# Performance work log

Hardware: AMD Instinct MI355X
Metric: run time of the kernel (lower is better)

## Reference

```python
import jax, jax.numpy as jnp
import numpy as np

D_MODEL = 1024
HEADS = 16
D_K = D_MODEL // HEADS
B, S = 2, 2048


def setup_inputs() -> dict:
    key = jax.random.key(0)
    ks = jax.random.split(key, 11)
    sc = 1.0 / np.sqrt(D_MODEL)
    return {
        "q": jax.random.normal(ks[0], (B, S, D_MODEL), jnp.float32),
        "k": jax.random.normal(ks[1], (B, S, D_MODEL), jnp.float32),
        "v": jax.random.normal(ks[2], (B, S, D_MODEL), jnp.float32),
        "Wq": jax.random.normal(ks[3], (D_MODEL, D_MODEL), jnp.float32) * sc,
        "bq": jnp.zeros((D_MODEL,), jnp.float32),
        "Wk": jax.random.normal(ks[4], (D_MODEL, D_MODEL), jnp.float32) * sc,
        "bk": jnp.zeros((D_MODEL,), jnp.float32),
        "Wv": jax.random.normal(ks[5], (D_MODEL, D_MODEL), jnp.float32) * sc,
        "bv": jnp.zeros((D_MODEL,), jnp.float32),
        "Wo": jax.random.normal(ks[6], (D_MODEL, D_MODEL), jnp.float32) * sc,
        "bo": jnp.zeros((D_MODEL,), jnp.float32),
    }


def reference(q, k, v, Wq, bq, Wk, bk, Wv, bv, Wo, bo):
    bs = q.shape[0]
    # linear projections then split heads: [B,S,D] -> [B,H,S,Dk]
    def proj(x, W, b):
        y = x @ W.T + b
        return y.reshape(bs, -1, HEADS, D_K).transpose(0, 2, 1, 3)

    qh = proj(q, Wq, bq)
    kh = proj(k, Wk, bk)
    vh = proj(v, Wv, bv)
    # scores: [B,H,Sq,Sk] -- full attention matrix as in the original
    scores = jnp.einsum("bhqd,bhkd->bhqk", qh, kh) / jnp.sqrt(
        jnp.asarray(D_K, jnp.float32))
    attn = jax.nn.softmax(scores, axis=-1)
    # dropout is identity in eval/reference mode
    out = jnp.einsum("bhqk,bhkd->bhqd", attn, vh)
    concat = out.transpose(0, 2, 1, 3).reshape(bs, -1, D_MODEL)
    return concat @ Wo.T + bo
```

## Files before the change

kernel.cpp:

```cpp
#include <hip/hip_runtime.h>
#include <hip/hip_bf16.h>

typedef __attribute__((ext_vector_type(8))) short bf16x8;
typedef __attribute__((ext_vector_type(4))) float f32x4;
typedef __attribute__((ext_vector_type(16))) float f32x16;

#define DM   1024
#define SEQ  2048
#define NB   2
#define NH   16
#define MR   (NB*SEQ)

#define SMK  (MR*DM)
#define W1M  (DM*DM)

#define QSCALE 0.18033688011112042f

#define OFF_QB  ((size_t)0)
#define OFF_KB  ((size_t)SMK)
#define OFF_VB  ((size_t)(2*(size_t)SMK))
#define OFF_WQ  ((size_t)(3*(size_t)SMK))
#define OFF_WO  ((size_t)(3*(size_t)SMK + 3*(size_t)W1M))
#define OFF_QP  ((size_t)(3*(size_t)SMK + 4*(size_t)W1M))
#define OFF_KP  ((size_t)(4*(size_t)SMK + 4*(size_t)W1M))
#define OFF_VP  ((size_t)(5*(size_t)SMK + 4*(size_t)W1M))
#define OFF_CC  ((size_t)0)

__device__ __forceinline__ unsigned short f2bf(float f) {
  union { __hip_bfloat16 b; unsigned short u; } cv;
  cv.b = __float2bfloat16(f);
  return cv.u;
}

__device__ __forceinline__ unsigned int cvtpk_bf16(float lo, float hi) {
  unsigned int r;
  asm("v_cvt_pk_bf16_f32 %0, %1, %2" : "=v"(r) : "v"(lo), "v"(hi));
  return r;
}

__device__ __forceinline__ void plane32_swap(unsigned int& a, unsigned int& b) {
  asm("v_permlane32_swap_b32 %0, %1" : "+v"(a), "+v"(b));
}

__global__ __launch_bounds__(256) void cvt_all(const float* __restrict__ q,
                                               const float* __restrict__ k,
                                               const float* __restrict__ v,
                                               const float* __restrict__ wq,
                                               const float* __restrict__ wk,
                                               const float* __restrict__ wv,
                                               const float* __restrict__ wo,
                                               unsigned short* __restrict__ ws) {
  int i = blockIdx.x * 256 + threadIdx.x;
  const float* src;
  unsigned short* dst;
  int j;
  if (i < 3 * (SMK / 4)) {
    int z = i >> 20;
    j = i & ((SMK / 4) - 1);
    src = (z == 0) ? q : ((z == 1) ? k : v);
    dst = ws + OFF_QB + (size_t)z * SMK;
  } else {
    int i2 = i - 3 * (SMK / 4);
    int z = i2 >> 18;
    j = i2 & ((W1M / 4) - 1);
    src = (z == 0) ? wq : ((z == 1) ? wk : ((z == 2) ? wv : wo));
    dst = ws + OFF_WQ + (size_t)z * W1M;
  }
  float4 val = reinterpret_cast<const float4*>(src)[j];
  ushort4 o;
  o.x = f2bf(val.x); o.y = f2bf(val.y); o.z = f2bf(val.z); o.w = f2bf(val.w);
  reinterpret_cast<ushort4*>(dst)[j] = o;
}

__device__ __forceinline__ void gload_lds16(const void* g, void* l) {
  __builtin_amdgcn_global_load_lds(
      (const __attribute__((address_space(1))) unsigned int*)g,
      (__attribute__((address_space(3))) unsigned int*)l,
      16, 0, 0);
}

template<int BM, int BN, bool OUT_BF16, bool BIAS_ROW>
__device__ __forceinline__ void gemm_bt_body(unsigned short* __restrict__ As,
                                             unsigned short* __restrict__ Bs,
                                             const unsigned short* __restrict__ A,
                                             const unsigned short* __restrict__ Bt,
                                             const float* __restrict__ bias,
                                             void* __restrict__ Cv,
                                             int N, int K, float scale,
                                             int brow, int bcol) {
  constexpr int MREP = BM / 32;
  constexpr int NREP = BN / 32;
  constexpr int LPS  = BM / 64 + BN / 64;
  const int tid  = threadIdx.x;
  const int lane = tid & 63;
  const int w    = tid >> 6;
  const int wr   = w >> 1, wc = w & 1;

  f32x4 acc[MREP][NREP];
#pragma unroll
  for (int m = 0; m < MREP; m++)
#pragma unroll
    for (int n = 0; n < NREP; n++) acc[m][n] = (f32x4){0.f, 0.f, 0.f, 0.f};

  const int srow = lane >> 2;
  const int scol = (lane & 3) * 8;

  auto stage = [&](int buf, int k0) {
#pragma unroll
    for (int c = w; c < BM / 16; c += 4)
      gload_lds16(A + (size_t)(brow + c * 16 + srow) * K + k0 + scol,
                  (char*)As + (size_t)buf * BM * 64 + c * 1024);
#pragma unroll
    for (int c = w; c < BN / 16; c += 4)
      gload_lds16(Bt + (size_t)(bcol + c * 16 + srow) * K + k0 + scol,
                  (char*)Bs + (size_t)buf * BN * 64 + c * 1024);
  };

  stage(0, 0);
  stage(1, 32);

  const int nk = K / 32;
  const int lrow_a = wr * (BM / 2) + (lane & 15);
  const int lrow_b = wc * (BN / 2) + (lane & 15);
  const int lcol   = (lane >> 4) * 8;

  int b0 = 0;
  for (int kt = 0; kt < nk; ++kt) {
    if (kt + 1 < nk) {
      if constexpr (LPS == 4) asm volatile("s_waitcnt vmcnt(4)" ::: "memory");
      else                    asm volatile("s_waitcnt vmcnt(3)" ::: "memory");
    } else {
      asm volatile("s_waitcnt vmcnt(0)" ::: "memory");
    }
    __builtin_amdgcn_s_barrier();
    __builtin_amdgcn_sched_barrier(0);
    if (kt + 2 < nk) {
      int bn = b0 + 2; if (bn >= 3) bn -= 3;
      stage(bn, (kt + 2) * 32);
    }
    bf16x8 a[MREP], b[NREP];
#pragma unroll
    for (int m = 0; m < MREP; m++)
      a[m] = *(const bf16x8*)&As[(size_t)b0 * BM * 32 + (lrow_a + m * 16) * 32 + lcol];
#pragma unroll
    for (int n = 0; n < NREP; n++)
      b[n] = *(const bf16x8*)&Bs[(size_t)b0 * BN * 32 + (lrow_b + n * 16) * 32 + lcol];
    __builtin_amdgcn_s_setprio(1);
#pragma unroll
    for (int m = 0; m < MREP; m++)
#pragma unroll
      for (int n = 0; n < NREP; n++)
        acc[m][n] = __builtin_amdgcn_mfma_f32_16x16x32_bf16(a[m], b[n], acc[m][n], 0, 0, 0);
    __builtin_amdgcn_s_setprio(0);
    b0 = (b0 == 2) ? 0 : b0 + 1;
  }

  const int crow0 = brow + wr * (BM / 2);
  const int ccol0 = bcol + wc * (BN / 2);
  const int rsub  = (lane >> 4) * 4;
  const int csub  = lane & 15;
#pragma unroll
  for (int m = 0; m < MREP; m++)
#pragma unroll
    for (int n = 0; n < NREP; n++) {
      int col = ccol0 + n * 16 + csub;
      float bcol_v = BIAS_ROW ? 0.f : bias[col];
#pragma unroll
      for (int qq = 0; qq < 4; qq++) {
        int row = crow0 + m * 16 + rsub + qq;
        float bb = BIAS_ROW ? bias[row] : bcol_v;
        float v = (acc[m][n][qq] + bb) * scale;
        if (OUT_BF16)
          ((unsigned short*)Cv)[(size_t)row * N + col] = f2bf(v);
        else
          ((float*)Cv)[(size_t)row * N + col] = v;
      }
    }
}

__global__ __launch_bounds__(256) void gemm_qkv(unsigned short* ws,
                                                const float* __restrict__ bq,
                                                const float* __restrict__ bk,
                                                const float* __restrict__ bv) {
  __shared__ unsigned short As[3 * 128 * 32];
  __shared__ unsigned short Bs[3 * 128 * 32];
  const int i  = blockIdx.x;
  const int x  = i & 7;
  const int r  = i >> 3;
  const int pm = r >> 3;
  const int bx = r & 7;
  const int p  = x * 12 + pm;
  const int z  = p >> 5;
  const int by = p & 31;
  if (z < 2) {
    gemm_bt_body<128, 128, true, false>(
        As, Bs,
        ws + OFF_QB + (size_t)z * SMK, ws + OFF_WQ + (size_t)z * W1M,
        z ? bk : bq, ws + OFF_QP + (size_t)z * SMK,
        DM, DM, z ? 1.f : QSCALE, by * 128, bx * 128);
  } else {
    gemm_bt_body<128, 128, true, true>(
        As, Bs,
        ws + OFF_WQ + 2 * W1M, ws + OFF_VB,
        bv, ws + OFF_VP,
        MR, DM, 1.f, bx * 128, by * 128);
  }
}

__global__ __launch_bounds__(256) void gemm_out(const unsigned short* __restrict__ ws,
                                                const float* __restrict__ bo,
                                                float* __restrict__ out) {
  __shared__ unsigned short As[3 * 64 * 32];
  __shared__ unsigned short Bs[3 * 128 * 32];
  const int i  = blockIdx.x;
  const int x  = i & 7;
  const int r  = i >> 3;
  const int pm = r >> 3;
  const int bx = r & 7;
  const int by = x * 8 + pm;
  gemm_bt_body<64, 128, false, false>(
      As, Bs,
      ws + OFF_CC, ws + OFF_WO, bo, out,
      DM, DM, 1.f, by * 64, bx * 128);
}

__global__ __launch_bounds__(512, 4) void flash_attn(unsigned short* ws) {
  __shared__ __align__(16) unsigned char smem[65536];

  const int tid  = threadIdx.x;
  const int lane = tid & 63;
  const int w    = tid >> 6;
  const int s    = w >> 2;
  const int wsub = w & 3;
  const int q    = lane & 31;
  const int hi   = lane >> 5;
  const int swq  = q & 7;
  const int bid  = blockIdx.x;
  const int swzb = (bid & 7) * 64 + (bid >> 3);
  const int qblk = swzb & 15;
  const int bh   = swzb >> 4;
  const int b    = bh >> 4, h = bh & 15;

  const unsigned short* Qp = ws + OFF_QP;
  const unsigned short* Kp = ws + OFF_KP;
  const unsigned short* Vp = ws + OFF_VP;
  unsigned short* CC = ws + OFF_CC;

  const unsigned short* Kg = Kp + (size_t)(b * SEQ) * DM + h * 64;
  const unsigned short* Vg = Vp + (size_t)(h * 64) * MR + (size_t)b * SEQ;

  bf16x8 bqf[4];
  {
    const unsigned short* qrow =
        Qp + (size_t)(b * SEQ + qblk * 128 + wsub * 32 + q) * DM + h * 64;
#pragma unroll
    for (int c = 0; c < 4; c++)
      bqf[c] = *(const bf16x8*)(qrow + c * 16 + hi * 8);
  }

  const bf16x8 kOnes = {16256, 16256, 16256, 16256, 16256, 16256, 16256, 16256};

  f32x16 o_acc[2];
  f32x16 o_l;
#pragma unroll
  for (int r = 0; r < 16; r++) o_l[r] = 0.f;
#pragma unroll
  for (int dt = 0; dt < 2; dt++)
#pragma unroll
    for (int r = 0; r < 16; r++) o_acc[dt][r] = 0.f;

  auto stage = [&](int buf, int t) {
    const unsigned short* Kt = Kg + (size_t)(s * 16 + t) * 64 * DM;
    const unsigned short* Vt = Vg + (s * 16 + t) * 64;
    char* base = (char*)smem + (size_t)(s * 2 + buf) * 16384;
#pragma unroll
    for (int i = 0; i < 2; i++) {
      int slot = wsub * 128 + i * 64 + lane;
      int srow = slot >> 3;
      int gch  = (slot & 7) ^ (srow & 7);
      gload_lds16(Kt + (size_t)srow * DM + gch * 8, base + slot * 16);
      gload_lds16(Vt + (size_t)srow * MR + gch * 8, base + 8192 + slot * 16);
    }
  };

  stage(0, 0);

  for (int t = 0; t < 16; ++t) {
    int buf = t & 1;
    __syncthreads();
    if (t + 1 < 16) stage(buf ^ 1, t + 1);
    const unsigned short* Kb = (const unsigned short*)(smem + (size_t)(s * 2 + buf) * 16384);
    const unsigned short* Vb = Kb + 4096;

    f32x16 st0, st1;
#pragma unroll
    for (int r = 0; r < 16; r++) { st0[r] = 0.f; st1[r] = 0.f; }
    __builtin_amdgcn_s_setprio(1);
#pragma unroll
    for (int c = 0; c < 4; c++) {
      int ch = (((c << 1) | hi) ^ swq) << 3;
      bf16x8 ak0 = *(const bf16x8*)&Kb[q * 64 + ch];
      bf16x8 ak1 = *(const bf16x8*)&Kb[(32 + q) * 64 + ch];
      st0 = __builtin_amdgcn_mfma_f32_32x32x16_bf16(ak0, bqf[c], st0, 0, 0, 0);
      st1 = __builtin_amdgcn_mfma_f32_32x32x16_bf16(ak1, bqf[c], st1, 0, 0, 0);
    }
    __builtin_amdgcn_s_setprio(0);

    unsigned int pk0[8], pk1[8];
#pragma unroll
    for (int p = 0; p < 8; p++) {
      float a0 = __builtin_amdgcn_exp2f(st0[2 * p]);
      float a1 = __builtin_amdgcn_exp2f(st0[2 * p + 1]);
      float b0 = __builtin_amdgcn_exp2f(st1[2 * p]);
      float b1 = __builtin_amdgcn_exp2f(st1[2 * p + 1]);
      pk0[p] = cvtpk_bf16(a0, a1);
      pk1[p] = cvtpk_bf16(b0, b1);
    }

    plane32_swap(pk0[0], pk0[2]); plane32_swap(pk0[1], pk0[3]);
    plane32_swap(pk0[4], pk0[6]); plane32_swap(pk0[5], pk0[7]);
    plane32_swap(pk1[0], pk1[2]); plane32_swap(pk1[1], pk1[3]);
    plane32_swap(pk1[4], pk1[6]); plane32_swap(pk1[5], pk1[7]);

    __builtin_amdgcn_s_setprio(1);
#pragma unroll
    for (int t4 = 0; t4 < 4; t4++) {
      union { unsigned int u[4]; bf16x8 v; } pb;
      const unsigned int* src = (t4 < 2) ? pk0 : pk1;
      pb.u[0] = src[(t4 & 1) * 4 + 0];
      pb.u[1] = src[(t4 & 1) * 4 + 1];
      pb.u[2] = src[(t4 & 1) * 4 + 2];
      pb.u[3] = src[(t4 & 1) * 4 + 3];
      int ch = (((t4 << 1) | hi) ^ swq) << 3;
      o_l = __builtin_amdgcn_mfma_f32_32x32x16_bf16(kOnes, pb.v, o_l, 0, 0, 0);
#pragma unroll
      for (int dt = 0; dt < 2; dt++) {
        bf16x8 av = *(const bf16x8*)&Vb[(dt * 32 + q) * 64 + ch];
        o_acc[dt] = __builtin_amdgcn_mfma_f32_32x32x16_bf16(av, pb.v, o_acc[dt], 0, 0, 0);
      }
    }
    __builtin_amdgcn_s_setprio(0);
  }

  __syncthreads();
  float* scr = (float*)smem;
  float lsum = o_l[0];
  if (s == 1) {
    int idx = (wsub * 64 + lane) * 33;
#pragma unroll
    for (int dt = 0; dt < 2; dt++)
#pragma unroll
      for (int r = 0; r < 16; r++) scr[idx + dt * 16 + r] = o_acc[dt][r];
    scr[idx + 32] = lsum;
  }
  __syncthreads();
  if (s == 0) {
    int idx = (wsub * 64 + lane) * 33;
#pragma unroll
    for (int dt = 0; dt < 2; dt++)
#pragma unroll
      for (int r = 0; r < 16; r++) o_acc[dt][r] += scr[idx + dt * 16 + r];
    float l = lsum + scr[idx + 32];
    float inv = 1.f / l;

    int qg = b * SEQ + qblk * 128 + wsub * 32 + q;
    unsigned short* crow = CC + (size_t)qg * DM + h * 64;
#pragma unroll
    for (int dt = 0; dt < 2; dt++)
#pragma unroll
      for (int rq = 0; rq < 4; rq++) {
        ushort4 o;
        o.x = f2bf(o_acc[dt][4 * rq + 0] * inv);
        o.y = f2bf(o_acc[dt][4 * rq + 1] * inv);
        o.z = f2bf(o_acc[dt][4 * rq + 2] * inv);
        o.w = f2bf(o_acc[dt][4 * rq + 3] * inv);
        *(ushort4*)&crow[dt * 32 + rq * 8 + hi * 4] = o;
      }
  }
}

extern "C" void kernel_launch(void* const* d_in, const int* in_sizes, int n_in,
                              void* d_out, int out_size, void* d_ws, size_t ws_size,
                              hipStream_t stream) {
  const float* q  = (const float*)d_in[0];
  const float* k  = (const float*)d_in[1];
  const float* v  = (const float*)d_in[2];
  const float* Wq = (const float*)d_in[3];
  const float* bq = (const float*)d_in[4];
  const float* Wk = (const float*)d_in[5];
  const float* bk = (const float*)d_in[6];
  const float* Wv = (const float*)d_in[7];
  const float* bv = (const float*)d_in[8];
  const float* Wo = (const float*)d_in[9];
  const float* bo = (const float*)d_in[10];

  unsigned short* ws = (unsigned short*)d_ws;
  float* out = (float*)d_out;

  cvt_all<<<dim3((3 * (SMK / 4) + 4 * (W1M / 4)) / 256), dim3(256), 0, stream>>>(
      q, k, v, Wq, Wk, Wv, Wo, ws);

  gemm_qkv<<<dim3(768), dim3(256), 0, stream>>>(ws, bq, bk, bv);

  flash_attn<<<dim3(512), dim3(512), 0, stream>>>(ws);

  gemm_out<<<dim3(512), dim3(256), 0, stream>>>(ws, bo, out);
}
```

Before: 117.5 us.

## Single-buffer attention K/V through registers and compute row sums with VALU

Replaces the double-buffered direct global-to-LDS K/V staging with register prefetch into a single LDS buffer, then commits it after a second barrier. This roughly halves shared memory use so launch bounds can ask for 6 blocks per CU instead of 4. The ones-matrix MFMA that computed softmax row sums is replaced by scalar adds over the exponentials plus a cross-half shuffle, freeing MFMA cycles and the o_l accumulator registers. The cost is an extra barrier per tile, more VGPRs for the staged data, and less overlap between loads and compute.

```diff
diff --git a/kernel.cpp b/kernel.cpp
--- a/kernel.cpp
+++ b/kernel.cpp
@@ -224,8 +224,8 @@
       DM, DM, 1.f, by * 64, bx * 128);
 }
 
-__global__ __launch_bounds__(512, 4) void flash_attn(unsigned short* ws) {
-  __shared__ __align__(16) unsigned char smem[65536];
+__global__ __launch_bounds__(512, 6) void flash_attn(unsigned short* ws) {
+  __shared__ __align__(16) unsigned char smem[34816];
 
   const int tid  = threadIdx.x;
   const int lane = tid & 63;
@@ -258,39 +258,44 @@
       bqf[c] = *(const bf16x8*)(qrow + c * 16 + hi * 8);
   }
 
-  const bf16x8 kOnes = {16256, 16256, 16256, 16256, 16256, 16256, 16256, 16256};
-
   f32x16 o_acc[2];
-  f32x16 o_l;
-#pragma unroll
-  for (int r = 0; r < 16; r++) o_l[r] = 0.f;
 #pragma unroll
   for (int dt = 0; dt < 2; dt++)
 #pragma unroll
     for (int r = 0; r < 16; r++) o_acc[dt][r] = 0.f;
-
-  auto stage = [&](int buf, int t) {
+  float l_run = 0.f;
+
+  bf16x8 kst[2], vst[2];
+  int slot0 = wsub * 128 + lane;
+  int slot1 = slot0 + 64;
+  int sr0 = slot0 >> 3, gc0 = (slot0 & 7) ^ (sr0 & 7);
+  int sr1 = slot1 >> 3, gc1 = (slot1 & 7) ^ (sr1 & 7);
+  char* base = (char*)smem + (size_t)s * 16384;
+
+  auto issue = [&](int t) {
     const unsigned short* Kt = Kg + (size_t)(s * 16 + t) * 64 * DM;
     const unsigned short* Vt = Vg + (s * 16 + t) * 64;
-    char* base = (char*)smem + (size_t)(s * 2 + buf) * 16384;
-#pragma unroll
-    for (int i = 0; i < 2; i++) {
-      int slot = wsub * 128 + i * 64 + lane;
-      int srow = slot >> 3;
-      int gch  = (slot & 7) ^ (srow & 7);
-      gload_lds16(Kt + (size_t)srow * DM + gch * 8, base + slot * 16);
-      gload_lds16(Vt + (size_t)srow * MR + gch * 8, base + 8192 + slot * 16);
-    }
+    kst[0] = *(const bf16x8*)(Kt + (size_t)sr0 * DM + gc0 * 8);
+    kst[1] = *(const bf16x8*)(Kt + (size_t)sr1 * DM + gc1 * 8);
+    vst[0] = *(const bf16x8*)(Vt + (size_t)sr0 * MR + gc0 * 8);
+    vst[1] = *(const bf16x8*)(Vt + (size_t)sr1 * MR + gc1 * 8);
   };
-
-  stage(0, 0);
+  auto commit = [&]() {
+    *(bf16x8*)(base + slot0 * 16) = kst[0];
+    *(bf16x8*)(base + slot1 * 16) = kst[1];
+    *(bf16x8*)(base + 8192 + slot0 * 16) = vst[0];
+    *(bf16x8*)(base + 8192 + slot1 * 16) = vst[1];
+  };
+
+  issue(0);
+  commit();
+
+  const unsigned short* Kb = (const unsigned short*)base;
+  const unsigned short* Vb = Kb + 4096;
 
   for (int t = 0; t < 16; ++t) {
-    int buf = t & 1;
+    if (t + 1 < 16) issue(t + 1);
     __syncthreads();
-    if (t + 1 < 16) stage(buf ^ 1, t + 1);
-    const unsigned short* Kb = (const unsigned short*)(smem + (size_t)(s * 2 + buf) * 16384);
-    const unsigned short* Vb = Kb + 4096;
 
     f32x16 st0, st1;
 #pragma unroll
@@ -307,15 +312,18 @@
     __builtin_amdgcn_s_setprio(0);
 
     unsigned int pk0[8], pk1[8];
+    float lt = 0.f;
 #pragma unroll
     for (int p = 0; p < 8; p++) {
       float a0 = __builtin_amdgcn_exp2f(st0[2 * p]);
       float a1 = __builtin_amdgcn_exp2f(st0[2 * p + 1]);
       float b0 = __builtin_amdgcn_exp2f(st1[2 * p]);
       float b1 = __builtin_amdgcn_exp2f(st1[2 * p + 1]);
+      lt += (a0 + a1) + (b0 + b1);
       pk0[p] = cvtpk_bf16(a0, a1);
       pk1[p] = cvtpk_bf16(b0, b1);
     }
+    l_run += lt;
 
     plane32_swap(pk0[0], pk0[2]); plane32_swap(pk0[1], pk0[3]);
     plane32_swap(pk0[4], pk0[6]); plane32_swap(pk0[5], pk0[7]);
@@ -332,7 +340,6 @@
       pb.u[2] = src[(t4 & 1) * 4 + 2];
       pb.u[3] = src[(t4 & 1) * 4 + 3];
       int ch = (((t4 << 1) | hi) ^ swq) << 3;
-      o_l = __builtin_amdgcn_mfma_f32_32x32x16_bf16(kOnes, pb.v, o_l, 0, 0, 0);
 #pragma unroll
       for (int dt = 0; dt < 2; dt++) {
         bf16x8 av = *(const bf16x8*)&Vb[(dt * 32 + q) * 64 + ch];
@@ -340,11 +347,14 @@
       }
     }
     __builtin_amdgcn_s_setprio(0);
+
+    __syncthreads();
+    if (t + 1 < 16) commit();
   }
 
   __syncthreads();
   float* scr = (float*)smem;
-  float lsum = o_l[0];
+  float lsum = l_run + __shfl_xor(l_run, 32, 64);
   if (s == 1) {
     int idx = (wsub * 64 + lane) * 33;
 #pragma unroll
```

After: 241.3 us. 2.05x slower.
